# Kernel optimization log

Hardware: AMD Instinct MI355X
Metric: run time of the kernel (lower is better)

The kernel has to match this reference:

```python
import jax, jax.numpy as jnp
import numpy as np
import math

EMBED = 512
KDIM = 512
VDIM = 512
H = 8
HD = EMBED // H
N = 2048
L = 2048
B = 4


def setup_inputs() -> dict:
    key = jax.random.key(0)
    ks = jax.random.split(key, 14)
    s = 1.0 / math.sqrt(EMBED)
    return {
        "q": jax.random.normal(ks[0], (N, B, EMBED), jnp.float32),
        "k": jax.random.normal(ks[1], (L, B, KDIM), jnp.float32),
        "v": jax.random.normal(ks[2], (L, B, VDIM), jnp.float32),
        "pe1": jax.random.normal(ks[3], (B, N, 3), jnp.float32),
        "pe2": jax.random.normal(ks[4], (L, 3), jnp.float32),
        "Wq": jax.random.normal(ks[5], (EMBED, EMBED), jnp.float32) * s,
        "bq": jnp.zeros((EMBED,), jnp.float32),
        "Wk": jax.random.normal(ks[6], (EMBED, KDIM), jnp.float32) * s,
        "bk": jnp.zeros((EMBED,), jnp.float32),
        "Wv": jax.random.normal(ks[7], (EMBED, VDIM), jnp.float32) * s,
        "bv": jnp.zeros((EMBED,), jnp.float32),
        "Wo": jax.random.normal(ks[8], (EMBED, EMBED), jnp.float32) * s,
        "bo": jnp.zeros((EMBED,), jnp.float32),
    }


def reference(q, k, v, pe1, pe2, Wq, bq, Wk, bk, Wv, bv, Wo, bo):
    n, b, _ = q.shape
    l = k.shape[0]
    # projections (nn.Linear: x @ W.T + b)
    qp = q @ Wq.T + bq  # (n, b, E)
    kp = k @ Wk.T + bk  # (l, b, E)
    vp = v @ Wv.T + bv  # (l, b, E)
    # split heads -> (b, H, n, hd)
    qh = qp.reshape(n, b, H, HD).transpose(1, 2, 0, 3)
    kh = kp.reshape(l, b, H, HD).transpose(1, 2, 0, 3)
    vh = vp.reshape(l, b, H, HD).transpose(1, 2, 0, 3)
    # relative PE bias: (b, n, l), broadcast over heads
    pe_scores = jnp.einsum('bnc,lc->bnl', pe1, pe2)[:, None, :, :]
    scores = (jnp.einsum('bhnd,bhld->bhnl', qh, kh) + pe_scores) / math.sqrt(HD)
    attn = jax.nn.softmax(scores, axis=-1)
    out = jnp.einsum('bhnl,bhld->bhnd', attn, vh)  # (b, H, n, hd)
    out = out.transpose(2, 0, 1, 3).reshape(n, b, EMBED)
    return out @ Wo.T + bo
```

## Files before the change

### kernel.cpp

```cpp
#include <hip/hip_runtime.h>
#include <math.h>

#define EMBED 512
#define HDIM 64
#define NHEADS 8
#define SEQ_N 2048
#define SEQ_L 2048
#define BATCH 4
#define MROWS (SEQ_N*BATCH)
#define BE (BATCH*EMBED)

#define QSCALE 0.18033688f

typedef _Float16 f16;
typedef _Float16 half8 __attribute__((ext_vector_type(8)));
typedef _Float16 half4 __attribute__((ext_vector_type(4)));
typedef _Float16 half2v __attribute__((ext_vector_type(2)));
typedef float floatx4 __attribute__((ext_vector_type(4)));
typedef float floatx16 __attribute__((ext_vector_type(16)));

static __device__ inline float fast_exp2(float x) {
#if __has_builtin(__builtin_amdgcn_exp2f)
  return __builtin_amdgcn_exp2f(x);
#else
  return __expf(x * 0.69314718056f);
#endif
}

static __device__ inline half2v pk2(float a, float b) {
#if __has_builtin(__builtin_amdgcn_cvt_pkrtz)
  return __builtin_bit_cast(half2v, __builtin_amdgcn_cvt_pkrtz(a, b));
#else
  half2v o; o[0] = (f16)a; o[1] = (f16)b; return o;
#endif
}

static __device__ inline void gload16(const void* g, void* l) {
  __builtin_amdgcn_global_load_lds(
      (__attribute__((address_space(1))) void*)(g),
      (__attribute__((address_space(3))) void*)(l), 16, 0, 0);
}

__global__ __launch_bounds__(256) void cvt_all(const float* __restrict__ q,
                                               const float* __restrict__ k,
                                               const float* __restrict__ v,
                                               const float* __restrict__ Wq,
                                               const float* __restrict__ Wk,
                                               const float* __restrict__ Wv,
                                               const float* __restrict__ Wo,
                                               f16* __restrict__ qb, f16* __restrict__ kb,
                                               f16* __restrict__ vb, f16* __restrict__ Wb) {
  const long TOK = (long)MROWS * EMBED;
  const long WSZ = (long)EMBED * EMBED;
  int y = blockIdx.y;
  long i = ((long)blockIdx.x * 256 + threadIdx.x) * 4;
  if (y < 3) {
    if (i < TOK) {
      const float* s = y == 0 ? q : y == 1 ? k : v;
      f16* d = y == 0 ? qb : y == 1 ? kb : vb;
      float4 f = *reinterpret_cast<const float4*>(s + i);
      half4 o; o[0] = (f16)f.x; o[1] = (f16)f.y; o[2] = (f16)f.z; o[3] = (f16)f.w;
      *reinterpret_cast<half4*>(d + i) = o;
    }
  } else {
    if (i < 4 * WSZ) {
      int sel = (int)(i >> 18);
      long off = i & (WSZ - 1);
      const float* s = sel == 0 ? Wq : sel == 1 ? Wk : sel == 2 ? Wv : Wo;
      float4 f = *reinterpret_cast<const float4*>(s + off);
      half4 o; o[0] = (f16)f.x; o[1] = (f16)f.y; o[2] = (f16)f.z; o[3] = (f16)f.w;
      *reinterpret_cast<half4*>(Wb + i) = o;
    }
  }
}

#define TST 136
__global__ __launch_bounds__(256) void gemm_qkv(const f16* __restrict__ A0,
                                                const f16* __restrict__ A1,
                                                const f16* __restrict__ A2,
                                                const f16* __restrict__ W0,
                                                const f16* __restrict__ W1,
                                                const f16* __restrict__ W2,
                                                const float* __restrict__ b0,
                                                const float* __restrict__ b1,
                                                const float* __restrict__ b2,
                                                f16* __restrict__ C0, f16* __restrict__ C1,
                                                f16* __restrict__ C2t) {
  __shared__ alignas(16) f16 As[128 * 32];
  __shared__ alignas(16) f16 Bs[128 * 32];
  __shared__ alignas(16) f16 Ts[128 * TST];
  const int sel = blockIdx.y >> 2;
  const f16* A = sel == 0 ? A0 : sel == 1 ? A1 : A2;
  const f16* Bt = sel == 0 ? W0 : sel == 1 ? W1 : W2;
  const float* bias = sel == 0 ? b0 : sel == 1 ? b1 : b2;
  const float scl = sel == 0 ? QSCALE : 1.0f;
  const int tid = threadIdx.x;
  const int wave = tid >> 6, lane = tid & 63, quad = lane >> 4, l16 = lane & 15;
  const int wm = wave & 1, wn = wave >> 1;
  const long m0 = (long)blockIdx.x * 128;
  const long n0 = (long)(blockIdx.y & 3) * 128;
  floatx4 acc[4][4] = {};
  const int srow = lane >> 2;
  const int scol = (lane & 3) * 8;

  for (int k0 = 0; k0 < EMBED; k0 += 32) {
    __syncthreads();
    gload16(A + (m0 + wave * 32 + srow) * EMBED + k0 + scol, &As[(wave * 32) * 32]);
    gload16(A + (m0 + wave * 32 + 16 + srow) * EMBED + k0 + scol, &As[(wave * 32 + 16) * 32]);
    gload16(Bt + (n0 + wave * 32 + srow) * EMBED + k0 + scol, &Bs[(wave * 32) * 32]);
    gload16(Bt + (n0 + wave * 32 + 16 + srow) * EMBED + k0 + scol, &Bs[(wave * 32 + 16) * 32]);
    __syncthreads();
    half8 af[4], bf[4];
#pragma unroll
    for (int i = 0; i < 4; ++i)
      af[i] = *reinterpret_cast<const half8*>(&As[(wm * 64 + i * 16 + l16) * 32 + quad * 8]);
#pragma unroll
    for (int j = 0; j < 4; ++j)
      bf[j] = *reinterpret_cast<const half8*>(&Bs[(wn * 64 + j * 16 + l16) * 32 + quad * 8]);
#pragma unroll
    for (int i = 0; i < 4; ++i)
#pragma unroll
      for (int j = 0; j < 4; ++j)
        acc[i][j] = __builtin_amdgcn_mfma_f32_16x16x32_f16(af[i], bf[j], acc[i][j], 0, 0, 0);
  }

  if (sel == 2) {
#pragma unroll
    for (int i = 0; i < 4; ++i)
#pragma unroll
      for (int r = 0; r < 4; ++r) {
        int ltok = wm * 16 + i * 4 + quad;
#pragma unroll
        for (int j = 0; j < 4; ++j) {
          int col = wn * 64 + j * 16 + l16;
          float val = acc[i][j][r] + bias[n0 + col];
          Ts[col * TST + r * 32 + ltok] = (f16)val;
        }
      }
    __syncthreads();
    const long ltok0 = m0 >> 2;
    for (int e = tid; e < 512; e += 256) {
      int col = e >> 2, bq = e & 3;
      long gcol = n0 + col;
      long hh = gcol >> 6, dd = gcol & 63;
      const f16* src = &Ts[col * TST + bq * 32];
      f16* dst = C2t + ((((long)bq << 3) + hh) * 64 + dd) * 2048 + ltok0;
#pragma unroll
      for (int x = 0; x < 4; ++x)
        *reinterpret_cast<uint4*>(dst + x * 8) =
            *reinterpret_cast<const uint4*>(src + x * 8);
    }
  } else {
    f16* C = sel == 0 ? C0 : C1;
#pragma unroll
    for (int i = 0; i < 4; ++i)
#pragma unroll
      for (int r = 0; r < 4; ++r) {
        long row = m0 + wm * 64 + i * 16 + quad * 4 + r;
#pragma unroll
        for (int j = 0; j < 4; ++j) {
          long col = n0 + wn * 64 + j * 16 + l16;
          C[row * EMBED + col] = (f16)((acc[i][j][r] + bias[col]) * scl);
        }
      }
  }
}

__global__ __launch_bounds__(256) void gemm_out(const f16* __restrict__ A,
                                                const f16* __restrict__ Bt,
                                                const float* __restrict__ bias,
                                                float* __restrict__ C) {
  __shared__ alignas(16) f16 As[128 * 32];
  __shared__ alignas(16) f16 Bs[64 * 32];
  const int tid = threadIdx.x;
  const int wave = tid >> 6, lane = tid & 63, quad = lane >> 4, l16 = lane & 15;
  const long m0 = (long)blockIdx.x * 128;
  const long n0 = (long)blockIdx.y * 64;
  floatx4 acc[2][4] = {};
  const int srow = lane >> 2;
  const int scol = (lane & 3) * 8;

  for (int k0 = 0; k0 < EMBED; k0 += 32) {
    __syncthreads();
    gload16(A + (m0 + wave * 32 + srow) * EMBED + k0 + scol, &As[(wave * 32) * 32]);
    gload16(A + (m0 + wave * 32 + 16 + srow) * EMBED + k0 + scol, &As[(wave * 32 + 16) * 32]);
    gload16(Bt + (n0 + wave * 16 + srow) * EMBED + k0 + scol, &Bs[(wave * 16) * 32]);
    __syncthreads();
    half8 af[2], bf[4];
#pragma unroll
    for (int i = 0; i < 2; ++i)
      af[i] = *reinterpret_cast<const half8*>(&As[(wave * 32 + i * 16 + l16) * 32 + quad * 8]);
#pragma unroll
    for (int j = 0; j < 4; ++j)
      bf[j] = *reinterpret_cast<const half8*>(&Bs[(j * 16 + l16) * 32 + quad * 8]);
#pragma unroll
    for (int i = 0; i < 2; ++i)
#pragma unroll
      for (int j = 0; j < 4; ++j)
        acc[i][j] = __builtin_amdgcn_mfma_f32_16x16x32_f16(af[i], bf[j], acc[i][j], 0, 0, 0);
  }
#pragma unroll
  for (int i = 0; i < 2; ++i)
#pragma unroll
    for (int r = 0; r < 4; ++r) {
      long row = m0 + wave * 32 + i * 16 + quad * 4 + r;
#pragma unroll
      for (int j = 0; j < 4; ++j) {
        long col = n0 + j * 16 + l16;
        C[row * EMBED + col] = acc[i][j][r] + bias[col];
      }
    }
}

#define KST 88
#define VST 136
#define NCHUNK (SEQ_L / 128)
#define BUFE (128 * KST + 64 * VST)
__global__ __launch_bounds__(512, 4) void attn_flash(const f16* __restrict__ qp,
                                                     const f16* __restrict__ kp,
                                                     const f16* __restrict__ vt,
                                                     const float* __restrict__ pe1,
                                                     const float* __restrict__ pe2,
                                                     f16* __restrict__ ao) {
  __shared__ alignas(16) f16 smem[2 * BUFE];
  float* comb = reinterpret_cast<float*>(smem);
  const int tid = threadIdx.x, wave = tid >> 6, lane = tid & 63;
  const int m = lane & 31, h = lane >> 5;
  const int strip = wave & 3, half = wave >> 2;
  const int n0 = blockIdx.x * 128;
  const int b = blockIdx.y >> 3, hd = blockIdx.y & 7;
  const long headoff = (long)b * EMBED + hd * HDIM;
  const long vhead = (long)blockIdx.y * 64 * 2048;

  f16* Ks0 = smem;
  for (int c = tid; c < 1024; c += 512) {
    int r = c >> 3, col = (c & 7) * 8;
    *reinterpret_cast<uint4*>(&Ks0[r * KST + col]) =
        *reinterpret_cast<const uint4*>(qp + (long)(n0 + r) * BE + headoff + col);
  }
  {
    const uint4 z4 = {0, 0, 0, 0};
    const uint2 z2 = {0, 0};
    int r = tid >> 2, s = tid & 3;
#pragma unroll
    for (int bb = 0; bb < 2; ++bb) {
      f16* Kb = smem + bb * BUFE;
      if (s == 0) *reinterpret_cast<uint2*>(&Kb[r * KST + 68]) = z2;
      else if (s == 1) *reinterpret_cast<uint4*>(&Kb[r * KST + 72]) = z4;
      else if (s == 2) *reinterpret_cast<uint4*>(&Kb[r * KST + 80]) = z4;
    }
  }
  if (tid < 128) {
    long base = ((long)b * SEQ_N + n0 + tid) * 3;
    half4 v8;
    v8[0] = (f16)(pe1[base + 0] * QSCALE);
    v8[1] = (f16)(pe1[base + 1] * QSCALE);
    v8[2] = (f16)(pe1[base + 2] * QSCALE);
    v8[3] = (f16)0.f;
    *reinterpret_cast<half4*>(&Ks0[tid * KST + 64]) = v8;
  }
  __syncthreads();

  half8 qf[5];
#pragma unroll
  for (int e = 0; e < 5; ++e)
    qf[e] = *reinterpret_cast<const half8*>(&Ks0[(strip * 32 + m) * KST + e * 16 + h * 8]);
  __syncthreads();

  auto stage = [&](int l0, f16* KsD, f16* VtD) {
    for (int c = tid; c < 1024; c += 512) {
      int r = c >> 3, col = (c & 7) * 8;
      *reinterpret_cast<uint4*>(&KsD[r * KST + col]) =
          *reinterpret_cast<const uint4*>(kp + (long)(l0 + r) * BE + headoff + col);
      int rv = c >> 4, cv = (c & 15) * 8;
      *reinterpret_cast<uint4*>(&VtD[rv * VST + cv]) =
          *reinterpret_cast<const uint4*>(vt + vhead + (long)rv * 2048 + l0 + cv);
    }
    if (tid < 128) {
      long bb = (long)(l0 + tid) * 3;
      half4 p2;
      p2[0] = (f16)pe2[bb + 0]; p2[1] = (f16)pe2[bb + 1];
      p2[2] = (f16)pe2[bb + 2]; p2[3] = (f16)0.f;
      *reinterpret_cast<half4*>(&KsD[tid * KST + 64]) = p2;
    }
  };
  stage(0, smem, smem + 128 * KST);
  __syncthreads();

  floatx16 oacc[2] = {};
  float lpart = 0.f;

#pragma unroll 1
  for (int c = 0; c < NCHUNK; ++c) {
    if (c + 1 < NCHUNK) {
      f16* nb = smem + ((c + 1) & 1) * BUFE;
      stage((c + 1) * 128, nb, nb + 128 * KST);
    }
    const f16* Ks = smem + (c & 1) * BUFE;
    const f16* Vt = Ks + 128 * KST;
#pragma unroll
    for (int tt = 0; tt < 2; ++tt) {
      const int t = half * 2 + tt;
      floatx16 st = {};
#pragma unroll
      for (int e = 0; e < 5; ++e) {
        half8 kf = *reinterpret_cast<const half8*>(&Ks[(t * 32 + m) * KST + e * 16 + h * 8]);
        st = __builtin_amdgcn_mfma_f32_32x32x16_f16(kf, qf[e], st, 0, 0, 0);
      }
      float p[16];
#pragma unroll
      for (int r = 0; r < 16; ++r) {
        p[r] = fast_exp2(st[r]);
        lpart += p[r];
      }
#pragma unroll
      for (int s = 0; s < 4; ++s) {
        half2v u0 = pk2(p[4 * s + 0], p[4 * s + 1]);
        half2v u1 = pk2(p[4 * s + 2], p[4 * s + 3]);
        half4 bp;
        bp[0] = u0[0]; bp[1] = u0[1]; bp[2] = u1[0]; bp[3] = u1[1];
        int lcol = t * 32 + s * 8 + h * 4;
#pragma unroll
        for (int dt = 0; dt < 2; ++dt) {
          half4 vf = *reinterpret_cast<const half4*>(&Vt[(dt * 32 + m) * VST + lcol]);
          oacc[dt] = __builtin_amdgcn_mfma_f32_32x32x8f16(vf, bp, oacc[dt], 0, 0, 0);
        }
      }
    }
    __syncthreads();
  }

  lpart += __shfl_xor(lpart, 32);

  if (half == 1) {
    float* dst = comb + (strip * 64 + lane) * 33;
#pragma unroll
    for (int dt = 0; dt < 2; ++dt)
#pragma unroll
      for (int x = 0; x < 16; ++x) dst[dt * 16 + x] = oacc[dt][x];
    dst[32] = lpart;
  }
  __syncthreads();
  if (half == 0) {
    const float* src = comb + (strip * 64 + lane) * 33;
#pragma unroll
    for (int dt = 0; dt < 2; ++dt)
#pragma unroll
      for (int x = 0; x < 16; ++x) oacc[dt][x] += src[dt * 16 + x];
    float inv = 1.f / (lpart + src[32]);
    long qrow = n0 + strip * 32 + m;
#pragma unroll
    for (int dt = 0; dt < 2; ++dt)
#pragma unroll
      for (int g = 0; g < 4; ++g) {
        half4 o4;
#pragma unroll
        for (int x = 0; x < 4; ++x) o4[x] = (f16)(oacc[dt][4 * g + x] * inv);
        int d = dt * 32 + 8 * g + 4 * h;
        *reinterpret_cast<half4*>(ao + qrow * BE + headoff + d) = o4;
      }
  }
}

extern "C" void kernel_launch(void* const* d_in, const int* in_sizes, int n_in,
                              void* d_out, int out_size, void* d_ws, size_t ws_size,
                              hipStream_t stream) {
  const float* q   = (const float*)d_in[0];
  const float* k   = (const float*)d_in[1];
  const float* v   = (const float*)d_in[2];
  const float* pe1 = (const float*)d_in[3];
  const float* pe2 = (const float*)d_in[4];
  const float* Wq  = (const float*)d_in[5];
  const float* bq  = (const float*)d_in[6];
  const float* Wk  = (const float*)d_in[7];
  const float* bk  = (const float*)d_in[8];
  const float* Wv  = (const float*)d_in[9];
  const float* bv  = (const float*)d_in[10];
  const float* Wo  = (const float*)d_in[11];
  const float* bo  = (const float*)d_in[12];
  float* out = (float*)d_out;

  f16* ws = (f16*)d_ws;
  const long TOK = (long)MROWS * EMBED;
  const long WSZ = (long)EMBED * EMBED;
  f16* qb  = ws;
  f16* kb  = qb + TOK;
  f16* vb  = kb + TOK;
  f16* Wqb = vb + TOK;
  f16* Wkb = Wqb + WSZ;
  f16* Wvb = Wkb + WSZ;
  f16* Wob = Wvb + WSZ;
  f16* qpb = Wob + WSZ;
  f16* kpb = qpb + TOK;
  f16* vtb = kpb + TOK;
  f16* aob = vtb + TOK;

  cvt_all<<<dim3(4096, 4), 256, 0, stream>>>(q, k, v, Wq, Wk, Wv, Wo, qb, kb, vb, Wqb);

  gemm_qkv<<<dim3(MROWS / 128, 12), 256, 0, stream>>>(qb, kb, vb, Wqb, Wkb, Wvb,
                                                      bq, bk, bv, qpb, kpb, vtb);

  attn_flash<<<dim3(SEQ_N / 128, BATCH * NHEADS), 512, 0, stream>>>(qpb, kpb, vtb, pe1, pe2, aob);

  gemm_out<<<dim3(MROWS / 128, EMBED / 64), 256, 0, stream>>>(aob, Wob, bo, out);
}
```

Measured before the change: 206.3 us.

## Double-buffer GEMM shared tiles and write V transpose directly to global

Both projection GEMMs now keep two LDS buffers for the A and B tiles. The load for step k+1 is issued before the MFMAs for step k, with one barrier per iteration, so global-to-LDS latency can overlap with compute. The V-projection epilogue drops its LDS transpose buffer and scatters f16 results straight into the transposed global layout. That frees shared memory and a barrier, but the global stores become strided and uncoalesced. The correctness of the prefetch depends on the barrier waiting for the outstanding LDS-destination loads.

```diff
diff --git a/kernel.cpp b/kernel.cpp
--- a/kernel.cpp
+++ b/kernel.cpp
@@ -74,7 +74,6 @@
   }
 }
 
-#define TST 136
 __global__ __launch_bounds__(256) void gemm_qkv(const f16* __restrict__ A0,
                                                 const f16* __restrict__ A1,
                                                 const f16* __restrict__ A2,
@@ -86,9 +85,8 @@
                                                 const float* __restrict__ b2,
                                                 f16* __restrict__ C0, f16* __restrict__ C1,
                                                 f16* __restrict__ C2t) {
-  __shared__ alignas(16) f16 As[128 * 32];
-  __shared__ alignas(16) f16 Bs[128 * 32];
-  __shared__ alignas(16) f16 Ts[128 * TST];
+  __shared__ alignas(16) f16 As[2][128 * 32];
+  __shared__ alignas(16) f16 Bs[2][128 * 32];
   const int sel = blockIdx.y >> 2;
   const f16* A = sel == 0 ? A0 : sel == 1 ? A1 : A2;
   const f16* Bt = sel == 0 ? W0 : sel == 1 ? W1 : W2;
@@ -103,25 +101,32 @@
   const int srow = lane >> 2;
   const int scol = (lane & 3) * 8;
 
-  for (int k0 = 0; k0 < EMBED; k0 += 32) {
-    __syncthreads();
-    gload16(A + (m0 + wave * 32 + srow) * EMBED + k0 + scol, &As[(wave * 32) * 32]);
-    gload16(A + (m0 + wave * 32 + 16 + srow) * EMBED + k0 + scol, &As[(wave * 32 + 16) * 32]);
-    gload16(Bt + (n0 + wave * 32 + srow) * EMBED + k0 + scol, &Bs[(wave * 32) * 32]);
-    gload16(Bt + (n0 + wave * 32 + 16 + srow) * EMBED + k0 + scol, &Bs[(wave * 32 + 16) * 32]);
-    __syncthreads();
+  auto stage = [&](int k0, int buf) {
+    gload16(A + (m0 + wave * 32 + srow) * EMBED + k0 + scol, &As[buf][(wave * 32) * 32]);
+    gload16(A + (m0 + wave * 32 + 16 + srow) * EMBED + k0 + scol, &As[buf][(wave * 32 + 16) * 32]);
+    gload16(Bt + (n0 + wave * 32 + srow) * EMBED + k0 + scol, &Bs[buf][(wave * 32) * 32]);
+    gload16(Bt + (n0 + wave * 32 + 16 + srow) * EMBED + k0 + scol, &Bs[buf][(wave * 32 + 16) * 32]);
+  };
+
+  stage(0, 0);
+  __syncthreads();
+
+  for (int kk = 0; kk < 16; ++kk) {
+    if (kk + 1 < 16) stage((kk + 1) * 32, (kk + 1) & 1);
+    const int cb = kk & 1;
     half8 af[4], bf[4];
 #pragma unroll
     for (int i = 0; i < 4; ++i)
-      af[i] = *reinterpret_cast<const half8*>(&As[(wm * 64 + i * 16 + l16) * 32 + quad * 8]);
+      af[i] = *reinterpret_cast<const half8*>(&As[cb][(wm * 64 + i * 16 + l16) * 32 + quad * 8]);
 #pragma unroll
     for (int j = 0; j < 4; ++j)
-      bf[j] = *reinterpret_cast<const half8*>(&Bs[(wn * 64 + j * 16 + l16) * 32 + quad * 8]);
+      bf[j] = *reinterpret_cast<const half8*>(&Bs[cb][(wn * 64 + j * 16 + l16) * 32 + quad * 8]);
 #pragma unroll
     for (int i = 0; i < 4; ++i)
 #pragma unroll
       for (int j = 0; j < 4; ++j)
         acc[i][j] = __builtin_amdgcn_mfma_f32_16x16x32_f16(af[i], bf[j], acc[i][j], 0, 0, 0);
+    __syncthreads();
   }
 
   if (sel == 2) {
@@ -129,27 +134,16 @@
     for (int i = 0; i < 4; ++i)
 #pragma unroll
       for (int r = 0; r < 4; ++r) {
-        int ltok = wm * 16 + i * 4 + quad;
+        long row = m0 + wm * 64 + i * 16 + quad * 4 + r;
+        long bq = row & 3, ltok = row >> 2;
 #pragma unroll
         for (int j = 0; j < 4; ++j) {
-          int col = wn * 64 + j * 16 + l16;
-          float val = acc[i][j][r] + bias[n0 + col];
-          Ts[col * TST + r * 32 + ltok] = (f16)val;
+          long col = n0 + wn * 64 + j * 16 + l16;
+          long hh = col >> 6, dd = col & 63;
+          C2t[(((bq << 3) + hh) * 64 + dd) * 2048 + ltok] =
+              (f16)(acc[i][j][r] + bias[col]);
         }
       }
-    __syncthreads();
-    const long ltok0 = m0 >> 2;
-    for (int e = tid; e < 512; e += 256) {
-      int col = e >> 2, bq = e & 3;
-      long gcol = n0 + col;
-      long hh = gcol >> 6, dd = gcol & 63;
-      const f16* src = &Ts[col * TST + bq * 32];
-      f16* dst = C2t + ((((long)bq << 3) + hh) * 64 + dd) * 2048 + ltok0;
-#pragma unroll
-      for (int x = 0; x < 4; ++x)
-        *reinterpret_cast<uint4*>(dst + x * 8) =
-            *reinterpret_cast<const uint4*>(src + x * 8);
-    }
   } else {
     f16* C = sel == 0 ? C0 : C1;
 #pragma unroll
@@ -170,8 +164,8 @@
                                                 const f16* __restrict__ Bt,
                                                 const float* __restrict__ bias,
                                                 float* __restrict__ C) {
-  __shared__ alignas(16) f16 As[128 * 32];
-  __shared__ alignas(16) f16 Bs[64 * 32];
+  __shared__ alignas(16) f16 As[2][128 * 32];
+  __shared__ alignas(16) f16 Bs[2][64 * 32];
   const int tid = threadIdx.x;
   const int wave = tid >> 6, lane = tid & 63, quad = lane >> 4, l16 = lane & 15;
   const long m0 = (long)blockIdx.x * 128;
@@ -180,24 +174,31 @@
   const int srow = lane >> 2;
   const int scol = (lane & 3) * 8;
 
-  for (int k0 = 0; k0 < EMBED; k0 += 32) {
-    __syncthreads();
-    gload16(A + (m0 + wave * 32 + srow) * EMBED + k0 + scol, &As[(wave * 32) * 32]);
-    gload16(A + (m0 + wave * 32 + 16 + srow) * EMBED + k0 + scol, &As[(wave * 32 + 16) * 32]);
-    gload16(Bt + (n0 + wave * 16 + srow) * EMBED + k0 + scol, &Bs[(wave * 16) * 32]);
-    __syncthreads();
+  auto stage = [&](int k0, int buf) {
+    gload16(A + (m0 + wave * 32 + srow) * EMBED + k0 + scol, &As[buf][(wave * 32) * 32]);
+    gload16(A + (m0 + wave * 32 + 16 + srow) * EMBED + k0 + scol, &As[buf][(wave * 32 + 16) * 32]);
+    gload16(Bt + (n0 + wave * 16 + srow) * EMBED + k0 + scol, &Bs[buf][(wave * 16) * 32]);
+  };
+
+  stage(0, 0);
+  __syncthreads();
+
+  for (int kk = 0; kk < 16; ++kk) {
+    if (kk + 1 < 16) stage((kk + 1) * 32, (kk + 1) & 1);
+    const int cb = kk & 1;
     half8 af[2], bf[4];
 #pragma unroll
     for (int i = 0; i < 2; ++i)
-      af[i] = *reinterpret_cast<const half8*>(&As[(wave * 32 + i * 16 + l16) * 32 + quad * 8]);
+      af[i] = *reinterpret_cast<const half8*>(&As[cb][(wave * 32 + i * 16 + l16) * 32 + quad * 8]);
 #pragma unroll
     for (int j = 0; j < 4; ++j)
-      bf[j] = *reinterpret_cast<const half8*>(&Bs[(j * 16 + l16) * 32 + quad * 8]);
+      bf[j] = *reinterpret_cast<const half8*>(&Bs[cb][(j * 16 + l16) * 32 + quad * 8]);
 #pragma unroll
     for (int i = 0; i < 2; ++i)
 #pragma unroll
       for (int j = 0; j < 4; ++j)
         acc[i][j] = __builtin_amdgcn_mfma_f32_16x16x32_f16(af[i], bf[j], acc[i][j], 0, 0, 0);
+    __syncthreads();
   }
 #pragma unroll
   for (int i = 0; i < 2; ++i)
```

After: 221.2 us. +7.2%, slower.
